# Optimization experiments

Measured on AMD Instinct MI355X. Metric: run time of the kernel, lower is better.

The kernel has to match this reference:

```python
import jax, jax.numpy as jnp
import numpy as np

DIM = 512
NSLOTS = 8
ITERS = 3
EPS = 1e-8
LN_EPS = 1e-5
SCALE = DIM ** -0.5


def _ln(x, g, b):
    m = jnp.mean(x, axis=-1, keepdims=True)
    v = jnp.mean((x - m) ** 2, axis=-1, keepdims=True)
    return (x - m) / jnp.sqrt(v + LN_EPS) * g + b


def _gru(x, h, W_ih, W_hh, b_ih, b_hh):
    # PyTorch GRUCell, gate order r,z,n
    gi = x @ W_ih.T + b_ih
    gh = h @ W_hh.T + b_hh
    ir, iz, inn = jnp.split(gi, 3, axis=-1)
    hr, hz, hn = jnp.split(gh, 3, axis=-1)
    r = jax.nn.sigmoid(ir + hr)
    z = jax.nn.sigmoid(iz + hz)
    n = jnp.tanh(inn + r * hn)
    return (1.0 - z) * n + z * h


def _norm_attn(dots):
    # softmax over slot axis, then renormalize over token axis
    a = jax.nn.softmax(dots, axis=1)
    return a / (jnp.sum(a, axis=-1, keepdims=True) + EPS)


def setup_inputs() -> dict:
    key = jax.random.key(0)
    ks = jax.random.split(key, 16)
    b, na, ni = 32, 1024, 3136
    d, hd = DIM, DIM  # hidden_dim = max(dim, 128) = 512
    s = 0.02
    inp = {
        'inputs_audio': jax.random.normal(ks[0], (b, na, d), jnp.float32),
        'inputs_image': jax.random.normal(ks[1], (b, ni, d), jnp.float32),
        'slots_noise': jax.random.normal(ks[2], (b, NSLOTS, d), jnp.float32),
        'slots_mu': jax.random.normal(ks[3], (1, 1, d), jnp.float32),
        'slots_logsigma': jnp.zeros((1, 1, d), jnp.float32),
        'ln_in_g': jnp.ones((d,), jnp.float32), 'ln_in_b': jnp.zeros((d,), jnp.float32),
        'ln_slots_g': jnp.ones((d,), jnp.float32), 'ln_slots_b': jnp.zeros((d,), jnp.float32),
        'ln_ff_g': jnp.ones((d,), jnp.float32), 'ln_ff_b': jnp.zeros((d,), jnp.float32),
        'Wq': jax.random.normal(ks[4], (d, d), jnp.float32) * s, 'bq': jnp.zeros((d,), jnp.float32),
        'Wk': jax.random.normal(ks[5], (d, d), jnp.float32) * s, 'bk': jnp.zeros((d,), jnp.float32),
        'Wv': jax.random.normal(ks[6], (d, d), jnp.float32) * s, 'bv': jnp.zeros((d,), jnp.float32),
        'W_ih': jax.random.normal(ks[7], (3 * d, d), jnp.float32) * s,
        'W_hh': jax.random.normal(ks[8], (3 * d, d), jnp.float32) * s,
        'b_ih': jnp.zeros((3 * d,), jnp.float32), 'b_hh': jnp.zeros((3 * d,), jnp.float32),
        'W1': jax.random.normal(ks[9], (hd, d), jnp.float32) * s, 'b1': jnp.zeros((hd,), jnp.float32),
        'W2': jax.random.normal(ks[10], (d, hd), jnp.float32) * s, 'b2': jnp.zeros((d,), jnp.float32),
    }
    return inp


def reference(inputs_audio, inputs_image, slots_noise, slots_mu, slots_logsigma,
              ln_in_g, ln_in_b, ln_slots_g, ln_slots_b, ln_ff_g, ln_ff_b,
              Wq, bq, Wk, bk, Wv, bv, W_ih, W_hh, b_ih, b_hh, W1, b1, W2, b2):
    b, na, d = inputs_audio.shape
    slots0 = slots_mu + jnp.exp(slots_logsigma) * slots_noise  # [b, S, d]

    ia = _ln(inputs_audio, ln_in_g, ln_in_b)
    ii = _ln(inputs_image, ln_in_g, ln_in_b)
    k_a = ia @ Wk.T + bk
    v_a = ia @ Wv.T + bv
    k_i = ii @ Wk.T + bk
    v_i = ii @ Wv.T + bv

    def mlp(x):
        return jax.nn.relu(x @ W1.T + b1) @ W2.T + b2

    def step(slots, k, v):
        prev = slots
        sn = _ln(slots, ln_slots_g, ln_slots_b)
        q = sn @ Wq.T + bq
        dots = jnp.einsum('bid,bjd->bij', q, k) * SCALE
        attn = _norm_attn(dots)
        upd = jnp.einsum('bjd,bij->bid', v, attn)
        h = _gru(upd.reshape(-1, d), prev.reshape(-1, d), W_ih, W_hh, b_ih, b_hh)
        slots = h.reshape(b, -1, d)
        slots = slots + mlp(_ln(slots, ln_ff_g, ln_ff_b))
        return slots, q, attn

    slots_a, slots_i = slots0, slots0
    for _ in range(ITERS):
        slots_a, q_a, attn_a = step(slots_a, k_a, v_a)
        slots_i, q_i, attn_i = step(slots_i, k_i, v_i)

    cross_ai = _norm_attn(jnp.einsum('bid,bjd->bij', q_a, k_i) * SCALE)  # audio->image
    cross_ia = _norm_attn(jnp.einsum('bid,bjd->bij', q_i, k_a) * SCALE)  # image->audio

    return (slots_a, q_a, k_a, attn_a, cross_ia,
            slots_i, q_i, k_i, attn_i, cross_ai)
```

## Files before the change

kernel.cpp:

```cpp
#include <hip/hip_runtime.h>
#include <hip/hip_bf16.h>

#define DIM 512
#define EPS 1e-8f
#define LN_EPS 1e-5f
#define SCALE 0.04419417382415922f

typedef float f32x4 __attribute__((ext_vector_type(4)));
typedef __bf16 bf16;
typedef __bf16 bf16x8 __attribute__((ext_vector_type(8)));

typedef const __attribute__((address_space(1))) void gvoid;
typedef __attribute__((address_space(3))) void lvoid;

__device__ inline float bf2f_lo(unsigned u) { union { unsigned x; float f; } c; c.x = u << 16; return c.f; }
__device__ inline float bf2f_hi(unsigned u) { union { unsigned x; float f; } c; c.x = u & 0xffff0000u; return c.f; }

#define SBAR() do { __builtin_amdgcn_sched_barrier(0); \
                    __builtin_amdgcn_s_barrier(); \
                    __builtin_amdgcn_sched_barrier(0); } while (0)

__global__ __launch_bounds__(256) void k_stats_convert(
    const float* __restrict__ xa, const float* __restrict__ xi,
    bf16* __restrict__ xbfa, bf16* __restrict__ xbfi,
    float* __restrict__ sa, float* __restrict__ si, int MA)
{
  int row = blockIdx.x * 4 + (threadIdx.x >> 6);
  int lane = threadIdx.x & 63;
  bool isA = row < MA;
  int lrow = isA ? row : row - MA;
  const float* xr = (isA ? xa : xi) + (size_t)lrow * DIM;
  bf16* xbf = (isA ? xbfa : xbfi) + (size_t)lrow * DIM;
  float* stats = (isA ? sa : si) + (size_t)lrow * 2;
  float4 a = *(const float4*)(xr + lane * 8);
  float4 b = *(const float4*)(xr + lane * 8 + 4);
  float s  = a.x + a.y + a.z + a.w + b.x + b.y + b.z + b.w;
  float ss = a.x*a.x + a.y*a.y + a.z*a.z + a.w*a.w
           + b.x*b.x + b.y*b.y + b.z*b.z + b.w*b.w;
  for (int off = 32; off; off >>= 1) { s += __shfl_xor(s, off); ss += __shfl_xor(ss, off); }
  float mean = s * (1.0f / DIM);
  float var  = ss * (1.0f / DIM) - mean * mean;
  float rs   = rsqrtf(var + LN_EPS);
  if (lane == 0) { stats[0] = mean; stats[1] = rs; }
  union { bf16 h[8]; uint4 u; } cv;
  cv.h[0] = (bf16)a.x; cv.h[1] = (bf16)a.y; cv.h[2] = (bf16)a.z; cv.h[3] = (bf16)a.w;
  cv.h[4] = (bf16)b.x; cv.h[5] = (bf16)b.y; cv.h[6] = (bf16)b.z; cv.h[7] = (bf16)b.w;
  *(uint4*)(xbf + lane * 8) = cv.u;
}

__global__ __launch_bounds__(256) void k_stats512(
    const float* __restrict__ x, float* __restrict__ stats)
{
  int row = blockIdx.x * 4 + (threadIdx.x >> 6);
  int lane = threadIdx.x & 63;
  const float* xr = x + (size_t)row * DIM;
  float4 a = *(const float4*)(xr + lane * 8);
  float4 b = *(const float4*)(xr + lane * 8 + 4);
  float s  = a.x + a.y + a.z + a.w + b.x + b.y + b.z + b.w;
  float ss = a.x*a.x + a.y*a.y + a.z*a.z + a.w*a.w
           + b.x*b.x + b.y*b.y + b.z*b.z + b.w*b.w;
  for (int off = 32; off; off >>= 1) { s += __shfl_xor(s, off); ss += __shfl_xor(ss, off); }
  float mean = s * (1.0f / DIM);
  float rs   = rsqrtf(ss * (1.0f / DIM) - mean * mean + LN_EPS);
  if (lane == 0) { stats[row * 2] = mean; stats[row * 2 + 1] = rs; }
}

__global__ __launch_bounds__(64) void k_prep(
    const float* __restrict__ Wk, const float* __restrict__ bk,
    const float* __restrict__ Wv, const float* __restrict__ bv,
    const float* __restrict__ g_in, const float* __restrict__ b_in,
    const float* __restrict__ Wq, const float* __restrict__ bq,
    const float* __restrict__ g_s, const float* __restrict__ b_s,
    const float* __restrict__ W1, const float* __restrict__ b1,
    const float* __restrict__ g_f, const float* __restrict__ b_f,
    bf16* __restrict__ wbf, float* __restrict__ c1kv, float* __restrict__ c2kv,
    float* __restrict__ Wqp, float* __restrict__ cq1, float* __restrict__ cq2,
    float* __restrict__ W1p, float* __restrict__ cf1, float* __restrict__ cf2)
{
  int n = blockIdx.x; int lane = threadIdx.x;
  if (n < 1024) {
    const float* W = (n < DIM) ? (Wk + (size_t)n * DIM) : (Wv + (size_t)(n - DIM) * DIM);
    float bias = (n < DIM) ? bk[n] : bv[n - DIM];
    float s1 = 0.f, s2 = 0.f;
    union { bf16 h[8]; uint4 u; } cv;
#pragma unroll
    for (int j = 0; j < 8; ++j) {
      int d = lane * 8 + j;
      float w = W[d];
      float gw = g_in[d] * w;
      s1 += gw; s2 += b_in[d] * w;
      cv.h[j] = (bf16)gw;
    }
    *(uint4*)(wbf + (size_t)n * DIM + lane * 8) = cv.u;
    for (int off = 32; off; off >>= 1) { s1 += __shfl_xor(s1, off); s2 += __shfl_xor(s2, off); }
    if (lane == 0) { c1kv[n] = s1; c2kv[n] = s2 + bias; }
  } else {
    int m; const float* W; float bias; const float* g; const float* b;
    float* Wp; float* cc1; float* cc2;
    if (n < 1536) { m = n - 1024; W = Wq + (size_t)m * DIM; bias = bq[m]; g = g_s; b = b_s; Wp = Wqp; cc1 = cq1; cc2 = cq2; }
    else          { m = n - 1536; W = W1 + (size_t)m * DIM; bias = b1[m]; g = g_f; b = b_f; Wp = W1p; cc1 = cf1; cc2 = cf2; }
    float s1 = 0.f, s2 = 0.f;
    float arr[8];
#pragma unroll
    for (int j = 0; j < 8; ++j) {
      int d = lane * 8 + j;
      float w = W[d];
      float gw = g[d] * w;
      s1 += gw; s2 += b[d] * w;
      arr[j] = gw;
    }
    *(float4*)(Wp + (size_t)m * DIM + lane * 8)     = make_float4(arr[0], arr[1], arr[2], arr[3]);
    *(float4*)(Wp + (size_t)m * DIM + lane * 8 + 4) = make_float4(arr[4], arr[5], arr[6], arr[7]);
    for (int off = 32; off; off >>= 1) { s1 += __shfl_xor(s1, off); s2 += __shfl_xor(s2, off); }
    if (lane == 0) { cc1[m] = s1; cc2[m] = s2 + bias; }
  }
}

__global__ __launch_bounds__(256, 4) void k_kv_gemm(
    const bf16* __restrict__ xa, const bf16* __restrict__ xi,
    const bf16* __restrict__ wbf,
    const float* __restrict__ sa, const float* __restrict__ si,
    const float* __restrict__ c1, const float* __restrict__ c2,
    float* __restrict__ ka, float* __restrict__ ki,
    bf16* __restrict__ kba, bf16* __restrict__ kbi,
    bf16* __restrict__ va, bf16* __restrict__ vi,
    int nblkA, int nblkTot)
{
  __shared__ bf16 As[2][128 * 32];
  __shared__ bf16 Bs[2][128 * 32];
  const int t = threadIdx.x, wave = t >> 6, lane = t & 63;
  int bid = blockIdx.x;
  int rid = (bid & 7) * (nblkTot >> 3) + (bid >> 3);
  bool isA = rid < nblkA;
  int lrid = isA ? rid : rid - nblkA;
  const bf16* x = isA ? xa : xi;
  const float* stats = isA ? sa : si;
  float* kout = isA ? ka : ki;
  bf16* kbf = isA ? kba : kbi;
  bf16* vbf = isA ? va : vi;
  const int row0 = (lrid >> 3) * 128, col0 = (lrid & 7) * 128;
  f32x4 acc[4][4] = {};

  const int sr  = wave * 16 + (lane >> 2);
  const int sgl = ((lane & 3) ^ ((lane >> 3) & 3)) * 8;
  const bf16* asrc = x   + (size_t)(row0 + sr) * DIM + sgl;
  const bf16* bsrc = wbf + (size_t)(col0 + sr) * DIM + sgl;

  auto stage = [&](int buf, int k0) {
#pragma unroll
    for (int p = 0; p < 2; ++p) {
      __builtin_amdgcn_global_load_lds(
          (gvoid*)(asrc + (size_t)(p * 64) * DIM + k0),
          (lvoid*)((char*)&As[buf][0] + (p * 256 + wave * 64) * 16), 16, 0, 0);
      __builtin_amdgcn_global_load_lds(
          (gvoid*)(bsrc + (size_t)(p * 64) * DIM + k0),
          (lvoid*)((char*)&Bs[buf][0] + (p * 256 + wave * 64) * 16), 16, 0, 0);
    }
  };

  const int l15 = lane & 15, q16 = lane >> 4;
  const int wm = wave >> 1, wn = wave & 1;
  const int gpx = (q16 ^ ((l15 >> 1) & 3)) * 8;

  stage(0, 0);
  stage(1, 32);
  asm volatile("s_waitcnt vmcnt(4)" ::: "memory");
  SBAR();
  int cur = 0;
  for (int ks = 0; ks < 16; ++ks) {
    const bf16* Ab = &As[cur][0];
    const bf16* Bb = &Bs[cur][0];
    bf16x8 ax[4], bw[4];
#pragma unroll
    for (int mi = 0; mi < 4; ++mi)
      ax[mi] = *(const bf16x8*)(Ab + (wm * 64 + mi * 16 + l15) * 32 + gpx);
#pragma unroll
    for (int ni = 0; ni < 4; ++ni)
      bw[ni] = *(const bf16x8*)(Bb + (wn * 64 + ni * 16 + l15) * 32 + gpx);
    __builtin_amdgcn_s_setprio(1);
#pragma unroll
    for (int ni = 0; ni < 4; ++ni)
#pragma unroll
      for (int mi = 0; mi < 4; ++mi)
        acc[ni][mi] = __builtin_amdgcn_mfma_f32_16x16x32_bf16(bw[ni], ax[mi], acc[ni][mi], 0, 0, 0);
    __builtin_amdgcn_s_setprio(0);
    if (ks == 15) break;
    SBAR();
    if (ks < 14) {
      stage(cur, (ks + 2) * 32);
      asm volatile("s_waitcnt vmcnt(4)" ::: "memory");
    } else {
      asm volatile("s_waitcnt vmcnt(0)" ::: "memory");
    }
    SBAR();
    cur ^= 1;
  }

#pragma unroll
  for (int mi = 0; mi < 4; ++mi) {
    int row = row0 + wm * 64 + mi * 16 + l15;
    float2 st = *(const float2*)&stats[row * 2];
    float rs = st.y, rm = st.y * st.x;
#pragma unroll
    for (int ni = 0; ni < 4; ++ni) {
      int col = col0 + wn * 64 + ni * 16 + q16 * 4;
      float4 c1v = *(const float4*)&c1[col];
      float4 c2v = *(const float4*)&c2[col];
      f32x4 a = acc[ni][mi];
      float4 o;
      o.x = rs * a[0] - rm * c1v.x + c2v.x;
      o.y = rs * a[1] - rm * c1v.y + c2v.y;
      o.z = rs * a[2] - rm * c1v.z + c2v.z;
      o.w = rs * a[3] - rm * c1v.w + c2v.w;
      union { bf16 h[4]; uint2 u; } pk;
      pk.h[0] = (bf16)o.x; pk.h[1] = (bf16)o.y; pk.h[2] = (bf16)o.z; pk.h[3] = (bf16)o.w;
      if (col0 < DIM) {
        *(float4*)&kout[(size_t)row * DIM + col] = o;
        if (kbf) *(uint2*)&kbf[(size_t)row * DIM + col] = pk.u;
      } else {
        *(uint2*)&vbf[(size_t)row * DIM + (col - DIM)] = pk.u;
      }
    }
  }
}

__global__ __launch_bounds__(256) void k_f2bf(
    const float* __restrict__ in, bf16* __restrict__ out)
{
  size_t i = ((size_t)blockIdx.x * 256 + threadIdx.x) * 8;
  float4 a = *(const float4*)(in + i);
  float4 b = *(const float4*)(in + i + 4);
  union { bf16 h[8]; uint4 u; } cv;
  cv.h[0] = (bf16)a.x; cv.h[1] = (bf16)a.y; cv.h[2] = (bf16)a.z; cv.h[3] = (bf16)a.w;
  cv.h[4] = (bf16)b.x; cv.h[5] = (bf16)b.y; cv.h[6] = (bf16)b.z; cv.h[7] = (bf16)b.w;
  *(uint4*)(out + i) = cv.u;
}

__global__ __launch_bounds__(256) void k_init_slots(
    const float* __restrict__ noise, const float* __restrict__ mu,
    const float* __restrict__ lsig, float* __restrict__ slots,
    float* __restrict__ stats)
{
  int row = blockIdx.x;
  int t = threadIdx.x;
  int d1 = t + 256;
  float v0 = mu[t]  + expf(lsig[t])  * noise[row * DIM + t];
  float v1 = mu[d1] + expf(lsig[d1]) * noise[row * DIM + d1];
  slots[(size_t)row * DIM + t]  = v0;
  slots[(size_t)row * DIM + d1] = v1;
  slots[131072 + (size_t)row * DIM + t]  = v0;
  slots[131072 + (size_t)row * DIM + d1] = v1;
  float s = v0 + v1, ss = v0 * v0 + v1 * v1;
  for (int off = 32; off; off >>= 1) { s += __shfl_xor(s, off); ss += __shfl_xor(ss, off); }
  __shared__ float red[8];
  int wv = t >> 6, ln = t & 63;
  if (ln == 0) { red[wv] = s; red[4 + wv] = ss; }
  __syncthreads();
  if (t == 0) {
    s = red[0] + red[1] + red[2] + red[3];
    ss = red[4] + red[5] + red[6] + red[7];
    float mean = s * (1.0f / DIM);
    float rs = rsqrtf(ss * (1.0f / DIM) - mean * mean + LN_EPS);
    stats[row * 2] = mean; stats[row * 2 + 1] = rs;
    stats[(row + 256) * 2] = mean; stats[(row + 256) * 2 + 1] = rs;
  }
}

template <int MODE>
__global__ __launch_bounds__(128) void k_sgemm(
    const float* __restrict__ A, const float* __restrict__ B, int N,
    float* __restrict__ C,
    const float* __restrict__ c1a, const float* __restrict__ c2a,
    const float* __restrict__ stats,
    const float* __restrict__ bias, const float* __restrict__ invden,
    const float* __restrict__ R,
    float* __restrict__ outA, float* __restrict__ outI,
    bf16* __restrict__ qbf)
{
  __shared__ float As[32][33];
  __shared__ float Bs[64][33];
  int t = threadIdx.x;
  int m0 = blockIdx.y * 32, n0 = blockIdx.x * 64;
  float acc[4][4] = {};
  for (int k0 = 0; k0 < DIM; k0 += 32) {
    __syncthreads();
#pragma unroll
    for (int p = 0; p < 2; ++p) {
      int idx = p * 128 + t, r = idx >> 3, c4 = (idx & 7) * 4;
      float4 v = *(const float4*)(A + (size_t)(m0 + r) * DIM + k0 + c4);
      As[r][c4] = v.x; As[r][c4 + 1] = v.y; As[r][c4 + 2] = v.z; As[r][c4 + 3] = v.w;
    }
#pragma unroll
    for (int p = 0; p < 4; ++p) {
      int idx = p * 128 + t, r = idx >> 3, c4 = (idx & 7) * 4;
      float4 v = *(const float4*)(B + (size_t)(n0 + r) * DIM + k0 + c4);
      Bs[r][c4] = v.x; Bs[r][c4 + 1] = v.y; Bs[r][c4 + 2] = v.z; Bs[r][c4 + 3] = v.w;
    }
    __syncthreads();
    int tr = t >> 4, tc = t & 15;
#pragma unroll
    for (int k = 0; k < 32; ++k) {
      float a0 = As[tr * 4][k], a1 = As[tr * 4 + 1][k], a2 = As[tr * 4 + 2][k], a3 = As[tr * 4 + 3][k];
      float b0 = Bs[tc * 4][k], b1 = Bs[tc * 4 + 1][k], b2 = Bs[tc * 4 + 2][k], b3 = Bs[tc * 4 + 3][k];
      acc[0][0] += a0 * b0; acc[0][1] += a0 * b1; acc[0][2] += a0 * b2; acc[0][3] += a0 * b3;
      acc[1][0] += a1 * b0; acc[1][1] += a1 * b1; acc[1][2] += a1 * b2; acc[1][3] += a1 * b3;
      acc[2][0] += a2 * b0; acc[2][1] += a2 * b1; acc[2][2] += a2 * b2; acc[2][3] += a2 * b3;
      acc[3][0] += a3 * b0; acc[3][1] += a3 * b1; acc[3][2] += a3 * b2; acc[3][3] += a3 * b3;
    }
  }
  int tr = t >> 4, tc = t & 15;
#pragma unroll
  for (int mi = 0; mi < 4; ++mi) {
    int row = m0 + tr * 4 + mi;
#pragma unroll
    for (int ni = 0; ni < 4; ++ni) {
      int col = n0 + tc * 4 + ni;
      float v = acc[mi][ni];
      if (MODE == 0 || MODE == 3) {
        float mean = stats[row * 2], rs = stats[row * 2 + 1];
        v = rs * v - rs * mean * c1a[col] + c2a[col];
      }
      if (MODE == 4) v += bias[col];
      if (MODE == 3) v = fmaxf(v, 0.0f);
      if (MODE == 4) v += R[(size_t)row * N + col];
      if (MODE == 0) {
        if (outA) {
          if (row < 256) outA[(size_t)row * DIM + col] = v;
          else           outI[(size_t)(row - 256) * DIM + col] = v;
        }
        qbf[(size_t)row * DIM + col] = (bf16)(v * SCALE);
      } else {
        C[(size_t)row * N + col] = v;
        if (MODE == 4 && outA) {
          if (row < 256) outA[(size_t)row * DIM + col] = v;
          else           outI[(size_t)(row - 256) * DIM + col] = v;
        }
      }
    }
  }
}

__global__ __launch_bounds__(128) void k_gates(
    const float* __restrict__ num, const float* __restrict__ slots,
    const float* __restrict__ Wih, const float* __restrict__ Whh,
    const float* __restrict__ bih, const float* __restrict__ bhh,
    const float* __restrict__ invden,
    float* __restrict__ gib, float* __restrict__ ghb)
{
  bool first = blockIdx.x < 24;
  const float* A = first ? num : slots;
  const float* B = first ? Wih : Whh;
  const float* bias = first ? bih : bhh;
  float* C = first ? gib : ghb;
  int n0 = (first ? blockIdx.x : blockIdx.x - 24) * 64;
  int m0 = blockIdx.y * 32;
  __shared__ float As[32][33];
  __shared__ float Bs[64][33];
  int t = threadIdx.x;
  float acc[4][4] = {};
  for (int k0 = 0; k0 < DIM; k0 += 32) {
    __syncthreads();
#pragma unroll
    for (int p = 0; p < 2; ++p) {
      int idx = p * 128 + t, r = idx >> 3, c4 = (idx & 7) * 4;
      float4 v = *(const float4*)(A + (size_t)(m0 + r) * DIM + k0 + c4);
      As[r][c4] = v.x; As[r][c4 + 1] = v.y; As[r][c4 + 2] = v.z; As[r][c4 + 3] = v.w;
    }
#pragma unroll
    for (int p = 0; p < 4; ++p) {
      int idx = p * 128 + t, r = idx >> 3, c4 = (idx & 7) * 4;
      float4 v = *(const float4*)(B + (size_t)(n0 + r) * DIM + k0 + c4);
      Bs[r][c4] = v.x; Bs[r][c4 + 1] = v.y; Bs[r][c4 + 2] = v.z; Bs[r][c4 + 3] = v.w;
    }
    __syncthreads();
    int tr = t >> 4, tc = t & 15;
#pragma unroll
    for (int k = 0; k < 32; ++k) {
      float a0 = As[tr * 4][k], a1 = As[tr * 4 + 1][k], a2 = As[tr * 4 + 2][k], a3 = As[tr * 4 + 3][k];
      float b0 = Bs[tc * 4][k], b1 = Bs[tc * 4 + 1][k], b2 = Bs[tc * 4 + 2][k], b3 = Bs[tc * 4 + 3][k];
      acc[0][0] += a0 * b0; acc[0][1] += a0 * b1; acc[0][2] += a0 * b2; acc[0][3] += a0 * b3;
      acc[1][0] += a1 * b0; acc[1][1] += a1 * b1; acc[1][2] += a1 * b2; acc[1][3] += a1 * b3;
      acc[2][0] += a2 * b0; acc[2][1] += a2 * b1; acc[2][2] += a2 * b2; acc[2][3] += a2 * b3;
      acc[3][0] += a3 * b0; acc[3][1] += a3 * b1; acc[3][2] += a3 * b2; acc[3][3] += a3 * b3;
    }
  }
  int tr = t >> 4, tc = t & 15;
#pragma unroll
  for (int mi = 0; mi < 4; ++mi) {
    int row = m0 + tr * 4 + mi;
    float sc = first ? invden[row] : 1.0f;
#pragma unroll
    for (int ni = 0; ni < 4; ++ni) {
      int col = n0 + tc * 4 + ni;
      C[(size_t)row * 1536 + col] = acc[mi][ni] * sc + bias[col];
    }
  }
}

template <int LAST>
__global__ __launch_bounds__(256) void k_dots_upd(
    const bf16* __restrict__ qA, const bf16* __restrict__ qI,
    const bf16* __restrict__ kA, const bf16* __restrict__ kI,
    const bf16* __restrict__ vA, const bf16* __restrict__ vI,
    float* __restrict__ aoutA, float* __restrict__ aoutI,
    float* __restrict__ acA, float* __restrict__ acI,
    float* __restrict__ denp, float* __restrict__ denpc,
    float* __restrict__ numpA, float* __restrict__ numpI,
    int NA_, int NI_)
{
  __shared__ bf16 ks[2][128 * 64];
  __shared__ float ash[128 * 12];
  __shared__ float dsh[64];
  int t = threadIdx.x, wave = t >> 6, lane = t & 63;
  int b = blockIdx.y, tile = blockIdx.x;
  bool isA = tile < 8;
  int til = isA ? tile : tile - 8;
  int N = isA ? NA_ : NI_;
  int nc = isA ? 8 : 25;
  int j0 = til * 128;
  const bf16* qo = (isA ? qA : qI) + (size_t)b * 8 * DIM;
  const bf16* qc = (isA ? qI : qA) + (size_t)b * 8 * DIM;
  const bf16* k  = (isA ? kA : kI) + (size_t)b * N * DIM;
  const bf16* v  = (isA ? vA : vI) + (size_t)b * N * DIM;
  float* aout = (isA ? aoutA : aoutI) + (LAST ? (size_t)b * 8 * N : 0);
  float* aco  = (isA ? acA  : acI ) + (LAST ? (size_t)b * 8 * N : 0);
  int drow = (isA ? 0 : 256) + b * 8;

  const int l15 = lane & 15, q16 = lane >> 4;
  bf16x8 afq[16], afqc[16];
  {
    const bf16* qr = qo + (size_t)(l15 & 7) * DIM + q16 * 8;
#pragma unroll
    for (int f = 0; f < 16; ++f) afq[f] = *(const bf16x8*)(qr + f * 32);
  }
  if (LAST) {
    const bf16* qr = qc + (size_t)(l15 & 7) * DIM + q16 * 8;
#pragma unroll
    for (int f = 0; f < 16; ++f) afqc[f] = *(const bf16x8*)(qr + f * 32);
  }

  const int sr  = wave * 8 + (lane >> 3);
  const int sgl = ((lane & 7) ^ (lane >> 3)) * 8;
  int jr = j0 + sr; if (jr > N - 1) jr = N - 1;
  const bf16* ksrc = k + (size_t)jr * DIM + sgl;
  int jr2 = j0 + 32 + sr; if (jr2 > N - 1) jr2 = N - 1;
  const bf16* ksrc2 = k + (size_t)jr2 * DIM + sgl;
  int jr3 = j0 + 64 + sr; if (jr3 > N - 1) jr3 = N - 1;
  const bf16* ksrc3 = k + (size_t)jr3 * DIM + sgl;
  int jr4 = j0 + 96 + sr; if (jr4 > N - 1) jr4 = N - 1;
  const bf16* ksrc4 = k + (size_t)jr4 * DIM + sgl;

  auto stage = [&](int buf, int c) {
    __builtin_amdgcn_global_load_lds((gvoid*)(ksrc  + c * 64),
        (lvoid*)((char*)&ks[0][0] + buf * 16384 + (0 * 256 + wave * 64) * 16), 16, 0, 0);
    __builtin_amdgcn_global_load_lds((gvoid*)(ksrc2 + c * 64),
        (lvoid*)((char*)&ks[0][0] + buf * 16384 + (1 * 256 + wave * 64) * 16), 16, 0, 0);
    __builtin_amdgcn_global_load_lds((gvoid*)(ksrc3 + c * 64),
        (lvoid*)((char*)&ks[0][0] + buf * 16384 + (2 * 256 + wave * 64) * 16), 16, 0, 0);
    __builtin_amdgcn_global_load_lds((gvoid*)(ksrc4 + c * 64),
        (lvoid*)((char*)&ks[0][0] + buf * 16384 + (3 * 256 + wave * 64) * 16), 16, 0, 0);
  };

  stage(0, 0);
  stage(1, 1);
  asm volatile("s_waitcnt vmcnt(4)" ::: "memory");
  SBAR();
  f32x4 acc[2] = {}, accc[2] = {};
  int cur = 0;
  for (int c = 0; c < 8; ++c) {
    const bf16* kb = &ks[0][0] + cur * (128 * 64);
    __builtin_amdgcn_s_setprio(1);
#pragma unroll
    for (int kk = 0; kk < 2; ++kk) {
#pragma unroll
      for (int n = 0; n < 2; ++n) {
        int R = wave * 32 + n * 16 + l15;
        int gp = (kk * 4 + q16) ^ (R & 7);
        bf16x8 bfr = *(const bf16x8*)(kb + R * 64 + gp * 8);
        acc[n] = __builtin_amdgcn_mfma_f32_16x16x32_bf16(afq[c * 2 + kk], bfr, acc[n], 0, 0, 0);
        if (LAST)
          accc[n] = __builtin_amdgcn_mfma_f32_16x16x32_bf16(afqc[c * 2 + kk], bfr, accc[n], 0, 0, 0);
      }
    }
    __builtin_amdgcn_s_setprio(0);
    if (c == 7) break;
    SBAR();
    if (c < 6) {
      stage(cur, c + 2);
      asm volatile("s_waitcnt vmcnt(4)" ::: "memory");
    } else {
      asm volatile("s_waitcnt vmcnt(0)" ::: "memory");
    }
    SBAR();
    cur ^= 1;
  }

  float dsum[8], dsumc[8];
#pragma unroll
  for (int i = 0; i < 8; ++i) { dsum[i] = 0.f; dsumc[i] = 0.f; }
#pragma unroll
  for (int n = 0; n < 2; ++n) {
    int jloc = wave * 32 + n * 16 + l15;
    int j = j0 + jloc;
    bool valid = (j < N);
    {
      float dv[8];
#pragma unroll
      for (int r = 0; r < 4; ++r) {
        float own = acc[n][r];
        float oth = __shfl_xor(own, 16);
        if (q16 == 0) { dv[r] = own; dv[4 + r] = oth; }
        else          { dv[r] = oth; dv[4 + r] = own; }
      }
      float mx = dv[0];
#pragma unroll
      for (int i = 1; i < 8; ++i) mx = fmaxf(mx, dv[i]);
      float sum = 0.f;
#pragma unroll
      for (int i = 0; i < 8; ++i) { dv[i] = __expf(dv[i] - mx); sum += dv[i]; }
      float inv = 1.0f / sum;
#pragma unroll
      for (int i = 0; i < 8; ++i) {
        float av = valid ? dv[i] * inv : 0.0f;
        dsum[i] += av;
        if (q16 == 0) {
          ash[jloc * 12 + i] = av;
          if (LAST && valid) aout[(size_t)i * N + j] = av;
        }
      }
    }
    if (LAST) {
      float dv[8];
#pragma unroll
      for (int r = 0; r < 4; ++r) {
        float own = accc[n][r];
        float oth = __shfl_xor(own, 16);
        if (q16 == 0) { dv[r] = own; dv[4 + r] = oth; }
        else          { dv[r] = oth; dv[4 + r] = own; }
      }
      float mx = dv[0];
#pragma unroll
      for (int i = 1; i < 8; ++i) mx = fmaxf(mx, dv[i]);
      float sum = 0.f;
#pragma unroll
      for (int i = 0; i < 8; ++i) { dv[i] = __expf(dv[i] - mx); sum += dv[i]; }
      float inv = 1.0f / sum;
#pragma unroll
      for (int i = 0; i < 8; ++i) {
        float av = valid ? dv[i] * inv : 0.0f;
        dsumc[i] += av;
        if (q16 == 0 && valid) aco[(size_t)i * N + j] = av;
      }
    }
  }
#pragma unroll
  for (int i = 0; i < 8; ++i) {
    float x1 = dsum[i];
    x1 += __shfl_xor(x1, 1); x1 += __shfl_xor(x1, 2);
    x1 += __shfl_xor(x1, 4); x1 += __shfl_xor(x1, 8);
    dsum[i] = x1;
    if (LAST) {
      float x2 = dsumc[i];
      x2 += __shfl_xor(x2, 1); x2 += __shfl_xor(x2, 2);
      x2 += __shfl_xor(x2, 4); x2 += __shfl_xor(x2, 8);
      dsumc[i] = x2;
    }
  }
  if (lane == 0) {
#pragma unroll
    for (int i = 0; i < 8; ++i) {
      dsh[wave * 8 + i] = dsum[i];
      if (LAST) dsh[32 + wave * 8 + i] = dsumc[i];
    }
  }
  __syncthreads();
  if (t < 8) {
    denp[((size_t)drow + t) * 32 + til] = dsh[t] + dsh[8 + t] + dsh[16 + t] + dsh[24 + t];
  }
  if (LAST && t >= 8 && t < 16) {
    int i = t - 8;
    denpc[((size_t)drow + i) * 32 + til] = dsh[32 + i] + dsh[40 + i] + dsh[48 + i] + dsh[56 + i];
  }

  int dg = t & 63, rg = t >> 6;
  float ua[8][8];
#pragma unroll
  for (int i = 0; i < 8; ++i)
#pragma unroll
    for (int j = 0; j < 8; ++j) ua[i][j] = 0.f;
  for (int jj = rg; jj < 128; jj += 4) {
    int jv = j0 + jj; if (jv > N - 1) jv = N - 1;
    uint4 vv = *(const uint4*)(v + (size_t)jv * DIM + dg * 8);
    float vf[8];
    vf[0] = bf2f_lo(vv.x); vf[1] = bf2f_hi(vv.x);
    vf[2] = bf2f_lo(vv.y); vf[3] = bf2f_hi(vv.y);
    vf[4] = bf2f_lo(vv.z); vf[5] = bf2f_hi(vv.z);
    vf[6] = bf2f_lo(vv.w); vf[7] = bf2f_hi(vv.w);
    float4 a0 = *(const float4*)&ash[jj * 12];
    float4 a1 = *(const float4*)&ash[jj * 12 + 4];
    float aw[8] = {a0.x, a0.y, a0.z, a0.w, a1.x, a1.y, a1.z, a1.w};
#pragma unroll
    for (int i = 0; i < 8; ++i)
#pragma unroll
      for (int j = 0; j < 8; ++j)
        ua[i][j] += aw[i] * vf[j];
  }
  float* red2 = (float*)&ks[0][0];
  float* np = (isA ? numpA : numpI) + (((size_t)b * nc + til) * 8) * DIM;
#pragma unroll
  for (int sg = 0; sg < 2; ++sg) {
    __syncthreads();
#pragma unroll
    for (int i4 = 0; i4 < 4; ++i4) {
      int i = sg * 4 + i4;
      *(float4*)&red2[(i4 * 4 + rg) * 512 + dg * 8]     = make_float4(ua[i][0], ua[i][1], ua[i][2], ua[i][3]);
      *(float4*)&red2[(i4 * 4 + rg) * 512 + dg * 8 + 4] = make_float4(ua[i][4], ua[i][5], ua[i][6], ua[i][7]);
    }
    __syncthreads();
    {
      int i4r = t >> 6;
      int d0r = (t & 63) * 8;
      float o[8];
#pragma unroll
      for (int j = 0; j < 8; ++j) {
        int d = d0r + j;
        o[j] = red2[(i4r * 4 + 0) * 512 + d] + red2[(i4r * 4 + 1) * 512 + d]
             + red2[(i4r * 4 + 2) * 512 + d] + red2[(i4r * 4 + 3) * 512 + d];
      }
      *(float4*)&np[(size_t)(sg * 4 + i4r) * DIM + d0r]     = make_float4(o[0], o[1], o[2], o[3]);
      *(float4*)&np[(size_t)(sg * 4 + i4r) * DIM + d0r + 4] = make_float4(o[4], o[5], o[6], o[7]);
    }
  }
}

__global__ __launch_bounds__(256) void k_numred(
    const float* __restrict__ numpA, const float* __restrict__ numpI,
    const float* __restrict__ denp,
    float* __restrict__ num, float* __restrict__ invden)
{
  int m = blockIdx.x, t = threadIdx.x;
  bool isA = m < 256;
  int mm = isA ? m : m - 256;
  int bb = mm >> 3, i = mm & 7;
  int nc = isA ? 8 : 25;
  const float* np = (isA ? numpA : numpI) + (((size_t)bb * nc) * 8 + i) * DIM;
  int d0 = t * 2;
  float s0 = 0.f, s1 = 0.f;
  for (int c = 0; c < nc; ++c) {
    float2 vv = *(const float2*)&np[(size_t)c * 8 * DIM + d0];
    s0 += vv.x; s1 += vv.y;
  }
  *(float2*)&num[(size_t)m * DIM + d0] = make_float2(s0, s1);
  if (t == 0) {
    float den = EPS;
    for (int c2 = 0; c2 < nc; ++c2) den += denp[(size_t)m * 32 + c2];
    invden[m] = 1.0f / den;
  }
}

__global__ __launch_bounds__(256) void k_gru(
    const float* __restrict__ gi, const float* __restrict__ gh,
    const float* __restrict__ prev,
    float* __restrict__ hout, float* __restrict__ stats_h)
{
  int m = blockIdx.x; int t = threadIdx.x;
  size_t b3 = (size_t)m * 1536, b1 = (size_t)m * DIM;
  float h[2]; float s = 0.f, ss = 0.f;
#pragma unroll
  for (int p = 0; p < 2; ++p) {
    int d = t + p * 256;
    float ir = gi[b3 + d], iz = gi[b3 + 512 + d], in_ = gi[b3 + 1024 + d];
    float hr = gh[b3 + d], hz = gh[b3 + 512 + d], hn = gh[b3 + 1024 + d];
    float r = 1.f / (1.f + __expf(-(ir + hr)));
    float z = 1.f / (1.f + __expf(-(iz + hz)));
    float n = tanhf(in_ + r * hn);
    float hv = (1.f - z) * n + z * prev[b1 + d];
    hout[b1 + d] = hv;
    h[p] = hv; s += hv; ss += hv * hv;
  }
  for (int off = 32; off; off >>= 1) { s += __shfl_xor(s, off); ss += __shfl_xor(ss, off); }
  __shared__ float red[8];
  int wv = t >> 6, ln = t & 63;
  if (ln == 0) { red[wv] = s; red[4 + wv] = ss; }
  __syncthreads();
  s = red[0] + red[1] + red[2] + red[3];
  ss = red[4] + red[5] + red[6] + red[7];
  float mean = s * (1.0f / DIM);
  float rs = rsqrtf(ss * (1.0f / DIM) - mean * mean + LN_EPS);
  if (t == 0) { stats_h[m * 2] = mean; stats_h[m * 2 + 1] = rs; }
}

__global__ __launch_bounds__(256) void k_renorm2(
    const float* __restrict__ aA, const float* __restrict__ aI,
    const float* __restrict__ acA, const float* __restrict__ acI,
    const float* __restrict__ denp, const float* __restrict__ denpc,
    float* __restrict__ oaA, float* __restrict__ oaI,
    float* __restrict__ ocIA, float* __restrict__ ocAI, int NA_, int NI_)
{
  int m = blockIdx.x; int t = threadIdx.x;
  bool cr = blockIdx.y != 0;
  bool isA = m < 256;
  int mm = isA ? m : m - 256;
  int N = isA ? NA_ : NI_;
  int nch = isA ? 8 : 25;
  const float* in = (cr ? (isA ? acA : acI) : (isA ? aA : aI)) + (size_t)mm * N;
  const float* dp = cr ? denpc : denp;
  float* out = (cr ? (isA ? ocIA : ocAI) : (isA ? oaA : oaI)) + (size_t)mm * N;
  float den = EPS;
  for (int c = 0; c < nch; ++c) den += dp[(size_t)m * 32 + c];
  float inv = 1.0f / den;
  for (int idx = t; idx * 4 < N; idx += 256) {
    float4 v = *(const float4*)&in[idx * 4];
    v.x *= inv; v.y *= inv; v.z *= inv; v.w *= inv;
    *(float4*)&out[idx * 4] = v;
  }
}

extern "C" void kernel_launch(void* const* d_in, const int* in_sizes, int n_in,
                              void* d_out, int out_size, void* d_ws, size_t ws_size,
                              hipStream_t stream)
{
  (void)in_sizes; (void)n_in; (void)out_size;
  const float* x_a   = (const float*)d_in[0];
  const float* x_i   = (const float*)d_in[1];
  const float* noise = (const float*)d_in[2];
  const float* mu    = (const float*)d_in[3];
  const float* lsig  = (const float*)d_in[4];
  const float* ln_in_g = (const float*)d_in[5];
  const float* ln_in_b = (const float*)d_in[6];
  const float* ln_s_g  = (const float*)d_in[7];
  const float* ln_s_b  = (const float*)d_in[8];
  const float* ln_f_g  = (const float*)d_in[9];
  const float* ln_f_b  = (const float*)d_in[10];
  const float* Wq = (const float*)d_in[11]; const float* bq = (const float*)d_in[12];
  const float* Wk = (const float*)d_in[13]; const float* bk = (const float*)d_in[14];
  const float* Wv = (const float*)d_in[15]; const float* bv = (const float*)d_in[16];
  const float* W_ih = (const float*)d_in[17]; const float* W_hh = (const float*)d_in[18];
  const float* b_ih = (const float*)d_in[19]; const float* b_hh = (const float*)d_in[20];
  const float* W1 = (const float*)d_in[21]; const float* b1 = (const float*)d_in[22];
  const float* W2 = (const float*)d_in[23]; const float* b2 = (const float*)d_in[24];

  const int NA = 1024, NI = 3136;
  const int MA = 32 * NA, MI = 32 * NI;

  float* out = (float*)d_out;
  float* o_slots_a  = out;
  float* o_q_a      = out + 131072;
  float* o_k_a      = out + 262144;
  float* o_attn_a   = out + 17039360;
  float* o_cross_ia = out + 17301504;
  float* o_slots_i  = out + 17563648;
  float* o_q_i      = out + 17694720;
  float* o_k_i      = out + 17825792;
  float* o_attn_i   = out + 69206016;
  float* o_cross_ai = out + 70008832;

  char* w = (char*)d_ws;
  size_t used = 0;
  auto alloc = [&](size_t bytes) {
    char* p = w + used;
    used += (bytes + 255) & ~(size_t)255;
    return p;
  };
  bf16* xbf_a = (bf16*)alloc((size_t)MA * DIM * 2);
  bf16* xbf_i = (bf16*)alloc((size_t)MI * DIM * 2);
  bf16* vbf_a = (bf16*)alloc((size_t)MA * DIM * 2);
  bf16* vbf_i = (bf16*)alloc((size_t)MI * DIM * 2);
  float* stats_a = (float*)alloc((size_t)MA * 2 * 4);
  float* stats_i = (float*)alloc((size_t)MI * 2 * 4);
  bf16* wbf  = (bf16*)alloc(1024 * 512 * 2);
  float* c1kv = (float*)alloc(1024 * 4);
  float* c2kv = (float*)alloc(1024 * 4);
  float* Wqp = (float*)alloc(512 * 512 * 4);
  float* cq1 = (float*)alloc(512 * 4);
  float* cq2 = (float*)alloc(512 * 4);
  float* W1p = (float*)alloc(512 * 512 * 4);
  float* cf1 = (float*)alloc(512 * 4);
  float* cf2 = (float*)alloc(512 * 4);
  float* slots = (float*)alloc(512 * 512 * 4);
  bf16*  qbf   = (bf16*)alloc(512 * 512 * 2);
  float* mid   = (float*)alloc(512 * 512 * 4);
  float* hid   = (float*)alloc(512 * 512 * 4);
  float* num   = (float*)alloc(512 * 512 * 4);
  float* gib   = (float*)alloc(512 * 1536 * 4);
  float* ghb   = (float*)alloc(512 * 1536 * 4);
  float* stats_s = (float*)alloc(512 * 2 * 4);
  float* stats_h = (float*)alloc(512 * 2 * 4);
  float* invden  = (float*)alloc(512 * 4);
  float* denp    = (float*)alloc(512 * 32 * 4);
  float* denpc   = (float*)alloc(512 * 32 * 4);
  float* abuf_a  = (float*)alloc((size_t)256 * NA * 4);
  float* abuf_i  = (float*)alloc((size_t)256 * NI * 4);
  float* abufc_a = (float*)alloc((size_t)256 * NA * 4);
  float* abufc_i = (float*)alloc((size_t)256 * NI * 4);
  float* numpA   = (float*)alloc((size_t)32 * 8 * 8 * DIM * 4);
  float* numpI   = (float*)alloc((size_t)32 * 25 * 8 * DIM * 4);
  if (used > ws_size) return;

  size_t kbf_bytes = (((size_t)MA * DIM * 2 + 255) & ~(size_t)255)
                   + (((size_t)MI * DIM * 2 + 255) & ~(size_t)255);
  bf16* kbf_a; bf16* kbf_i; bool kbf_fused;
  if (used + kbf_bytes <= ws_size) {
    kbf_a = (bf16*)alloc((size_t)MA * DIM * 2);
    kbf_i = (bf16*)alloc((size_t)MI * DIM * 2);
    kbf_fused = true;
  } else {
    kbf_a = xbf_a; kbf_i = xbf_i;
    kbf_fused = false;
  }

  k_stats_convert<<<(MA + MI) / 4, 256, 0, stream>>>(x_a, x_i, xbf_a, xbf_i,
                                                     stats_a, stats_i, MA);
  k_prep<<<2048, 64, 0, stream>>>(Wk, bk, Wv, bv, ln_in_g, ln_in_b,
                                  Wq, bq, ln_s_g, ln_s_b, W1, b1, ln_f_g, ln_f_b,
                                  wbf, c1kv, c2kv, Wqp, cq1, cq2, W1p, cf1, cf2);
  {
    int nblkA = (MA / 128) * 8;
    int nblkTot = nblkA + (MI / 128) * 8;
    k_kv_gemm<<<nblkTot, 256, 0, stream>>>(xbf_a, xbf_i, wbf, stats_a, stats_i,
        c1kv, c2kv, o_k_a, o_k_i,
        kbf_fused ? kbf_a : nullptr, kbf_fused ? kbf_i : nullptr,
        vbf_a, vbf_i, nblkA, nblkTot);
  }
  if (!kbf_fused) {
    k_f2bf<<<MA * DIM / 2048, 256, 0, stream>>>(o_k_a, kbf_a);
    k_f2bf<<<MI * DIM / 2048, 256, 0, stream>>>(o_k_i, kbf_i);
  }
  k_init_slots<<<256, 256, 0, stream>>>(noise, mu, lsig, slots, stats_s);

  for (int it = 0; it < 3; ++it) {
    bool last = (it == 2);
    k_sgemm<0><<<dim3(8, 16), 128, 0, stream>>>(slots, Wqp, DIM, nullptr,
        cq1, cq2, stats_s, nullptr, nullptr, nullptr,
        last ? o_q_a : nullptr, last ? o_q_i : nullptr, qbf);
    if (!last)
      k_dots_upd<0><<<dim3(33, 32), 256, 0, stream>>>(qbf, qbf + 256 * DIM,
          kbf_a, kbf_i, vbf_a, vbf_i,
          nullptr, nullptr, nullptr, nullptr, denp, nullptr,
          numpA, numpI, NA, NI);
    else
      k_dots_upd<1><<<dim3(33, 32), 256, 0, stream>>>(qbf, qbf + 256 * DIM,
          kbf_a, kbf_i, vbf_a, vbf_i,
          abuf_a, abuf_i, abufc_a, abufc_i, denp, denpc,
          numpA, numpI, NA, NI);
    k_numred<<<512, 256, 0, stream>>>(numpA, numpI, denp, num, invden);
    k_gates<<<dim3(48, 16), 128, 0, stream>>>(num, slots, W_ih, W_hh,
        b_ih, b_hh, invden, gib, ghb);
    k_gru<<<512, 256, 0, stream>>>(gib, ghb, slots, mid, stats_h);
    k_sgemm<3><<<dim3(8, 16), 128, 0, stream>>>(mid, W1p, DIM, hid,
        cf1, cf2, stats_h, nullptr, nullptr, nullptr, nullptr, nullptr, nullptr);
    k_sgemm<4><<<dim3(8, 16), 128, 0, stream>>>(hid, W2, DIM, slots,
        nullptr, nullptr, nullptr, b2, nullptr, mid,
        last ? o_slots_a : nullptr, last ? o_slots_i : nullptr, nullptr);
    if (!last) k_stats512<<<128, 256, 0, stream>>>(slots, stats_s);
  }

  k_renorm2<<<dim3(512, 2), 256, 0, stream>>>(abuf_a, abuf_i, abufc_a, abufc_i,
      denp, denpc, o_attn_a, o_attn_i, o_cross_ia, o_cross_ai, NA, NI);
}
```

Measured before the change: 1.103 ms.

## Pad bf16 K/V row stride and emit fp32 K via separate conversion pass

The bf16 K and V buffers get a padded row stride of 528 elements instead of 512, and the dots/update kernel indexes them with this stride. The aim is to avoid power-of-two strides that can map rows onto the same memory channels or banks. In the fused path the KV GEMM epilogue now writes only bf16 K. A new kernel then expands that bf16 K into the fp32 K output, which lightens the GEMM's store load. The cost is an extra launch and extra memory traffic, and the fp32 K output now carries bf16 rounding.

```diff
diff --git a/kernel.cpp b/kernel.cpp
--- a/kernel.cpp
+++ b/kernel.cpp
@@ -124,7 +124,7 @@
     float* __restrict__ ka, float* __restrict__ ki,
     bf16* __restrict__ kba, bf16* __restrict__ kbi,
     bf16* __restrict__ va, bf16* __restrict__ vi,
-    int nblkA, int nblkTot)
+    int nblkA, int nblkTot, int kst)
 {
   __shared__ bf16 As[2][128 * 32];
   __shared__ bf16 Bs[2][128 * 32];
@@ -215,13 +215,28 @@
       union { bf16 h[4]; uint2 u; } pk;
       pk.h[0] = (bf16)o.x; pk.h[1] = (bf16)o.y; pk.h[2] = (bf16)o.z; pk.h[3] = (bf16)o.w;
       if (col0 < DIM) {
-        *(float4*)&kout[(size_t)row * DIM + col] = o;
-        if (kbf) *(uint2*)&kbf[(size_t)row * DIM + col] = pk.u;
+        if (kbf) *(uint2*)&kbf[(size_t)row * kst + col] = pk.u;
+        else     *(float4*)&kout[(size_t)row * DIM + col] = o;
       } else {
-        *(uint2*)&vbf[(size_t)row * DIM + (col - DIM)] = pk.u;
+        *(uint2*)&vbf[(size_t)row * kst + (col - DIM)] = pk.u;
       }
     }
   }
+}
+
+__global__ __launch_bounds__(256) void k_kbf2f(
+    const bf16* __restrict__ kba, const bf16* __restrict__ kbi,
+    float* __restrict__ oa, float* __restrict__ oi, int MA, int kst)
+{
+  int row = blockIdx.x * 4 + (threadIdx.x >> 6);
+  int lane = threadIdx.x & 63;
+  bool isA = row < MA;
+  int lr = isA ? row : row - MA;
+  const bf16* src = (isA ? kba : kbi) + (size_t)lr * kst + lane * 8;
+  float* dst = (isA ? oa : oi) + (size_t)lr * DIM + lane * 8;
+  uint4 u = *(const uint4*)src;
+  *(float4*)dst = make_float4(bf2f_lo(u.x), bf2f_hi(u.x), bf2f_lo(u.y), bf2f_hi(u.y));
+  *(float4*)(dst + 4) = make_float4(bf2f_lo(u.z), bf2f_hi(u.z), bf2f_lo(u.w), bf2f_hi(u.w));
 }
 
 __global__ __launch_bounds__(256) void k_f2bf(
@@ -406,7 +421,7 @@
     float* __restrict__ acA, float* __restrict__ acI,
     float* __restrict__ denp, float* __restrict__ denpc,
     float* __restrict__ numpA, float* __restrict__ numpI,
-    int NA_, int NI_)
+    int NA_, int NI_, int kst)
 {
   __shared__ bf16 ks[2][128 * 64];
   __shared__ float ash[128 * 12];
@@ -420,8 +435,8 @@
   int j0 = til * 128;
   const bf16* qo = (isA ? qA : qI) + (size_t)b * 8 * DIM;
   const bf16* qc = (isA ? qI : qA) + (size_t)b * 8 * DIM;
-  const bf16* k  = (isA ? kA : kI) + (size_t)b * N * DIM;
-  const bf16* v  = (isA ? vA : vI) + (size_t)b * N * DIM;
+  const bf16* k  = (isA ? kA : kI) + (size_t)b * N * kst;
+  const bf16* v  = (isA ? vA : vI) + (size_t)b * N * kst;
   float* aout = (isA ? aoutA : aoutI) + (LAST ? (size_t)b * 8 * N : 0);
   float* aco  = (isA ? acA  : acI ) + (LAST ? (size_t)b * 8 * N : 0);
   int drow = (isA ? 0 : 256) + b * 8;
@@ -442,13 +457,13 @@
   const int sr  = wave * 8 + (lane >> 3);
   const int sgl = ((lane & 7) ^ (lane >> 3)) * 8;
   int jr = j0 + sr; if (jr > N - 1) jr = N - 1;
-  const bf16* ksrc = k + (size_t)jr * DIM + sgl;
+  const bf16* ksrc = k + (size_t)jr * kst + sgl;
   int jr2 = j0 + 32 + sr; if (jr2 > N - 1) jr2 = N - 1;
-  const bf16* ksrc2 = k + (size_t)jr2 * DIM + sgl;
+  const bf16* ksrc2 = k + (size_t)jr2 * kst + sgl;
   int jr3 = j0 + 64 + sr; if (jr3 > N - 1) jr3 = N - 1;
-  const bf16* ksrc3 = k + (size_t)jr3 * DIM + sgl;
+  const bf16* ksrc3 = k + (size_t)jr3 * kst + sgl;
   int jr4 = j0 + 96 + sr; if (jr4 > N - 1) jr4 = N - 1;
-  const bf16* ksrc4 = k + (size_t)jr4 * DIM + sgl;
+  const bf16* ksrc4 = k + (size_t)jr4 * kst + sgl;
 
   auto stage = [&](int buf, int c) {
     __builtin_amdgcn_global_load_lds((gvoid*)(ksrc  + c * 64),
@@ -590,7 +605,7 @@
     for (int j = 0; j < 8; ++j) ua[i][j] = 0.f;
   for (int jj = rg; jj < 128; jj += 4) {
     int jv = j0 + jj; if (jv > N - 1) jv = N - 1;
-    uint4 vv = *(const uint4*)(v + (size_t)jv * DIM + dg * 8);
+    uint4 vv = *(const uint4*)(v + (size_t)jv * kst + dg * 8);
     float vf[8];
     vf[0] = bf2f_lo(vv.x); vf[1] = bf2f_hi(vv.x);
     vf[2] = bf2f_lo(vv.y); vf[3] = bf2f_hi(vv.y);
@@ -742,6 +757,7 @@
 
   const int NA = 1024, NI = 3136;
   const int MA = 32 * NA, MI = 32 * NI;
+  const int KST = 528;
 
   float* out = (float*)d_out;
   float* o_slots_a  = out;
@@ -764,8 +780,8 @@
   };
   bf16* xbf_a = (bf16*)alloc((size_t)MA * DIM * 2);
   bf16* xbf_i = (bf16*)alloc((size_t)MI * DIM * 2);
-  bf16* vbf_a = (bf16*)alloc((size_t)MA * DIM * 2);
-  bf16* vbf_i = (bf16*)alloc((size_t)MI * DIM * 2);
+  bf16* vbf_a = (bf16*)alloc((size_t)MA * KST * 2);
+  bf16* vbf_i = (bf16*)alloc((size_t)MI * KST * 2);
   float* stats_a = (float*)alloc((size_t)MA * 2 * 4);
   float* stats_i = (float*)alloc((size_t)MI * 2 * 4);
   bf16* wbf  = (bf16*)alloc(1024 * 512 * 2);
@@ -797,16 +813,16 @@
   float* numpI   = (float*)alloc((size_t)32 * 25 * 8 * DIM * 4);
   if (used > ws_size) return;
 
-  size_t kbf_bytes = (((size_t)MA * DIM * 2 + 255) & ~(size_t)255)
-                   + (((size_t)MI * DIM * 2 + 255) & ~(size_t)255);
-  bf16* kbf_a; bf16* kbf_i; bool kbf_fused;
+  size_t kbf_bytes = (((size_t)MA * KST * 2 + 255) & ~(size_t)255)
+                   + (((size_t)MI * KST * 2 + 255) & ~(size_t)255);
+  bf16* kbf_a; bf16* kbf_i; bool kbf_fused; int kst;
   if (used + kbf_bytes <= ws_size) {
-    kbf_a = (bf16*)alloc((size_t)MA * DIM * 2);
-    kbf_i = (bf16*)alloc((size_t)MI * DIM * 2);
-    kbf_fused = true;
+    kbf_a = (bf16*)alloc((size_t)MA * KST * 2);
+    kbf_i = (bf16*)alloc((size_t)MI * KST * 2);
+    kbf_fused = true; kst = KST;
   } else {
     kbf_a = xbf_a; kbf_i = xbf_i;
-    kbf_fused = false;
+    kbf_fused = false; kst = DIM;
   }
 
   k_stats_convert<<<(MA + MI) / 4, 256, 0, stream>>>(x_a, x_i, xbf_a, xbf_i,
@@ -820,9 +836,11 @@
     k_kv_gemm<<<nblkTot, 256, 0, stream>>>(xbf_a, xbf_i, wbf, stats_a, stats_i,
         c1kv, c2kv, o_k_a, o_k_i,
         kbf_fused ? kbf_a : nullptr, kbf_fused ? kbf_i : nullptr,
-        vbf_a, vbf_i, nblkA, nblkTot);
-  }
-  if (!kbf_fused) {
+        vbf_a, vbf_i, nblkA, nblkTot, kst);
+  }
+  if (kbf_fused) {
+    k_kbf2f<<<(MA + MI) / 4, 256, 0, stream>>>(kbf_a, kbf_i, o_k_a, o_k_i, MA, kst);
+  } else {
     k_f2bf<<<MA * DIM / 2048, 256, 0, stream>>>(o_k_a, kbf_a);
     k_f2bf<<<MI * DIM / 2048, 256, 0, stream>>>(o_k_i, kbf_i);
   }
@@ -837,12 +855,12 @@
       k_dots_upd<0><<<dim3(33, 32), 256, 0, stream>>>(qbf, qbf + 256 * DIM,
           kbf_a, kbf_i, vbf_a, vbf_i,
           nullptr, nullptr, nullptr, nullptr, denp, nullptr,
-          numpA, numpI, NA, NI);
+          numpA, numpI, NA, NI, kst);
     else
       k_dots_upd<1><<<dim3(33, 32), 256, 0, stream>>>(qbf, qbf + 256 * DIM,
           kbf_a, kbf_i, vbf_a, vbf_i,
           abuf_a, abuf_i, abufc_a, abufc_i, denp, denpc,
-          numpA, numpI, NA, NI);
+          numpA, numpI, NA, NI, kst);
     k_numred<<<512, 256, 0, stream>>>(numpA, numpI, denp, num, invden);
     k_gates<<<dim3(48, 16), 128, 0, stream>>>(num, slots, W_ih, W_hh,
         b_ih, b_hh, invden, gib, ghb);
```

Measured after the change: 1.115 ms. No clear change (+1.1%).
